# Kernel optimization log

Hardware: AMD Instinct MI355X
Metric: run time of the kernel (lower is better)

Reference implementation:

```python
import jax, jax.numpy as jnp
import numpy as np

B, N, D, H, DH = 4, 1024, 1024, 16, 64
INNER = H * DH  # 1024


def setup_inputs() -> dict:
    key = jax.random.key(0)
    k0, k1, k2, k3 = jax.random.split(key, 4)
    x = jax.random.normal(k0, (B, N, D), dtype=jnp.float32)
    # float 0/1 padding mask per token
    mask = jax.random.randint(k1, (B, N), 0, 2).astype(jnp.float32)
    w_qkv = jax.random.normal(k2, (D, 3 * INNER), dtype=jnp.float32) * (D ** -0.5)
    w_out = jax.random.normal(k3, (INNER, D), dtype=jnp.float32) * (INNER ** -0.5)
    b_out = jnp.zeros((D,), dtype=jnp.float32)
    return {"x": x, "mask": mask, "w_qkv": w_qkv, "w_out": w_out, "b_out": b_out}


def reference(x, mask, w_qkv, w_out, b_out):
    scale = DH ** -0.5
    qkv = x @ w_qkv  # [B,N,3*INNER]
    q, k, v = jnp.split(qkv, 3, axis=-1)
    resh = lambda t: t.reshape(B, N, H, DH).transpose(0, 2, 1, 3)  # b h n d
    q, k, v = resh(q), resh(k), resh(v)
    dots = jnp.einsum('bhnd,bhmd->bhnm', q, k) * scale  # [B,H,N,N]
    # attn_bias = 1 - m_i*m_j; blocked where isclose(attn_bias, 1) i.e. pair ~ 0
    pair = mask[:, None, :, None] * mask[:, None, None, :]  # [B,1,N,N]
    blocked = jnp.isclose(1.0 - pair, jnp.ones_like(pair))
    dots = jnp.where(blocked, -jnp.inf, dots)
    # fully-masked-row fixup: rows that are all -inf get dots=0, attn forced to 0
    valid = jnp.any(dots != -jnp.inf, axis=-1, keepdims=True)  # [B,H,N,1]
    dots = jnp.where(valid, dots, 0.0)
    attn = jax.nn.softmax(dots, axis=-1)
    attn = jnp.where(valid, attn, 0.0)
    out = jnp.einsum('bhnm,bhmd->bhnd', attn, v)
    out = out.transpose(0, 2, 1, 3).reshape(B, N, INNER)
    return out @ w_out + b_out
```

## Files before the change

kernel.cpp:

```cpp
#include <hip/hip_runtime.h>

#define INF __builtin_inff()

typedef __attribute__((ext_vector_type(8))) short bf16x8;
typedef __attribute__((ext_vector_type(4))) short s16x4;
typedef __attribute__((ext_vector_type(4))) float f32x4;
typedef __attribute__((ext_vector_type(8))) unsigned short u16x8;
typedef __attribute__((ext_vector_type(4))) unsigned short u16x4;

#define MFMA16(a, b, c) __builtin_amdgcn_mfma_f32_16x16x32_bf16(a, b, c, 0, 0, 0)

#define ASYNC16(g, l) __builtin_amdgcn_global_load_lds( \
    (const __attribute__((address_space(1))) unsigned int*)(const void*)(g), \
    (__attribute__((address_space(3))) unsigned int*)(void*)(l), 16, 0, 0)

__device__ __forceinline__ unsigned short f2bf(float f) {
  union { float f; unsigned u; } v; v.f = f;
  unsigned r = v.u + 0x7fffu + ((v.u >> 16) & 1u);
  return (unsigned short)(r >> 16);
}

__global__ __launch_bounds__(1024) void k_scan(
    const float* __restrict__ mask, unsigned short* __restrict__ perm, int* __restrict__ nv) {
  __shared__ int wsum[16];
  __shared__ int woff[16];
  const int b = blockIdx.x, t = threadIdx.x;
  const int wid = t >> 6, lane = t & 63;
  const bool valid = (mask[b * 1024 + t] != 0.f);
  unsigned long long bal = __ballot(valid);
  int pre = __popcll(bal & ((1ull << lane) - 1ull));
  if (lane == 0) wsum[wid] = __popcll(bal);
  __syncthreads();
  if (t < 16) { int s = 0; for (int i = 0; i < t; ++i) s += wsum[i]; woff[t] = s; }
  __syncthreads();
  const int nvt = woff[15] + wsum[15];
  const int p = woff[wid] + pre;
  perm[b * 1024 + (valid ? p : nvt + (t - p))] = (unsigned short)t;
  if (t == 0) nv[b] = nvt;
}

__global__ __launch_bounds__(256) void k_cvtg(
    const float* __restrict__ x, const unsigned short* __restrict__ perm,
    const int* __restrict__ nvb, unsigned short* __restrict__ xc) {
  const int id = blockIdx.x;
  const int b = id >> 10, slot = id & 1023;
  const int nv = nvb[b];
  if (slot >= ((nv + 127) & ~127)) return;
  const int t = threadIdx.x;
  u16x4 o;
  if (slot < nv) {
    int tok = perm[b * 1024 + slot];
    float4 f = ((const float4*)(x + ((size_t)(b * 1024 + tok)) * 1024))[t];
    o[0] = f2bf(f.x); o[1] = f2bf(f.y); o[2] = f2bf(f.z); o[3] = f2bf(f.w);
  } else {
    o[0] = o[1] = o[2] = o[3] = 0;
  }
  ((u16x4*)(xc + ((size_t)(b * 1024 + slot)) * 1024))[t] = o;
}

__global__ __launch_bounds__(256) void k_wtrans(
    const float* __restrict__ wqkv, const float* __restrict__ wout,
    unsigned short* __restrict__ wqkvt, unsigned short* __restrict__ woutt) {
  __shared__ float tile[32][33];
  int id = blockIdx.x;
  const float* src; unsigned short* dst; int C, bc, br;
  if (id < 3072) { src = wqkv;  dst = wqkvt; C = 3072; bc = (id % 96) * 32; br = (id / 96) * 32; }
  else { id -= 3072; src = wout; dst = woutt; C = 1024; bc = (id & 31) * 32; br = (id >> 5) * 32; }
  const int R = 1024;
  const int tx = threadIdx.x & 31, ty = threadIdx.x >> 5;
#pragma unroll
  for (int i = 0; i < 32; i += 8)
    tile[ty + i][tx] = src[(size_t)(br + ty + i) * C + bc + tx];
  __syncthreads();
#pragma unroll
  for (int i = 0; i < 32; i += 8)
    dst[(size_t)(bc + ty + i) * R + br + tx] = f2bf(tile[tx][ty + i]);
}

__global__ __launch_bounds__(256) void k_gemm_qkv(
    const unsigned short* __restrict__ A, const unsigned short* __restrict__ Bt,
    const int* __restrict__ nvb,
    unsigned short* __restrict__ qcmp, unsigned short* __restrict__ kcmp,
    unsigned short* __restrict__ vt) {
  __shared__ unsigned short SH[32768];
  const int lid = blockIdx.x;
  const int xcd = lid & 7, i6 = lid >> 3;
  const int colt = xcd * 3 + (i6 % 3);
  const int rowt = i6 / 3;
  const int b = rowt >> 3, mt = rowt & 7;
  const int nv = nvb[b];
  if (mt * 128 >= nv) return;
  const int bm0 = mt * 128;
  const int bn0 = colt * 128;
  const size_t abase = ((size_t)(b * 1024 + bm0)) * 1024;
  const int t = threadIdx.x;
  const int lane = t & 63, wave = t >> 6;
  const int wm = (wave >> 1) * 64, wn = (wave & 1) * 64;
  const int lr = lane & 15, quad = lane >> 4;
  const int sw = lr & 7;
  f32x4 acc[4][4] = {};
  auto stage = [&](int pp, int k0) {
    unsigned short* As = SH + pp * 16384;
    unsigned short* Bs = As + 8192;
#pragma unroll
    for (int j = 0; j < 4; ++j) {
      int idx = t + j * 256;
      int row = idx >> 3;
      int g = (idx ^ row) & 7;
      ASYNC16(&A[abase + (size_t)row * 1024 + k0 + g * 8], &As[idx * 8]);
      ASYNC16(&Bt[((size_t)(bn0 + row)) * 1024 + k0 + g * 8], &Bs[idx * 8]);
    }
  };
  stage(0, 0);
  for (int it = 0; it < 16; ++it) {
    const int pp = it & 1;
    __syncthreads();
    if (it + 1 < 16) stage(1 - pp, (it + 1) * 64);
    const unsigned short* As = SH + pp * 16384;
    const unsigned short* Bs = As + 8192;
#pragma unroll
    for (int ks = 0; ks < 2; ++ks) {
      bf16x8 af[4], bfr[4];
#pragma unroll
      for (int i = 0; i < 4; ++i)
        af[i] = *(const bf16x8*)(&As[(wm + i * 16 + lr) * 64 + (((ks * 4 + quad) ^ sw)) * 8]);
#pragma unroll
      for (int j = 0; j < 4; ++j)
        bfr[j] = *(const bf16x8*)(&Bs[(wn + j * 16 + lr) * 64 + (((ks * 4 + quad) ^ sw)) * 8]);
#pragma unroll
      for (int i = 0; i < 4; ++i)
#pragma unroll
        for (int j = 0; j < 4; ++j)
          acc[i][j] = MFMA16(af[i], bfr[j], acc[i][j]);
    }
  }
  const int sec = bn0 >> 10;
  const int js0 = bn0 & 1023;
#pragma unroll
  for (int hh = 0; hh < 2; ++hh) {
    __syncthreads();
    if ((wave >> 1) == hh) {
#pragma unroll
      for (int i = 0; i < 4; ++i)
#pragma unroll
        for (int j = 0; j < 4; ++j)
#pragma unroll
          for (int r = 0; r < 4; ++r)
            SH[(i * 16 + quad * 4 + r) * 136 + wn + j * 16 + lr] = f2bf(acc[i][j][r]);
    }
    __syncthreads();
    if (sec < 2) {
      unsigned short* dstT = sec ? kcmp : qcmp;
#pragma unroll
      for (int rr = 0; rr < 4; ++rr) {
        int lrow = (t >> 4) + rr * 16;
        int ck = t & 15;
        int slot = bm0 + hh * 64 + lrow;
        int js = js0 + ck * 8;
        int h = js >> 6, d = js & 63;
        u16x8 v = *(u16x8*)(&SH[lrow * 136 + ck * 8]);
        *(u16x8*)(&dstT[(((size_t)(b * 16 + h)) * 1024 + slot) * 64 + d]) = v;
      }
    } else {
      const int c = t & 127, seg = t >> 7;
      const int js = js0 + c, h = js >> 6, d = js & 63;
      unsigned short* vrow =
          &vt[(((size_t)(b * 16 + h)) * 64 + d) * 1024 + bm0 + hh * 64 + seg * 32];
#pragma unroll
      for (int s4 = 0; s4 < 4; ++s4) {
        u16x8 v;
#pragma unroll
        for (int s = 0; s < 8; ++s) v[s] = SH[(seg * 32 + s4 * 8 + s) * 136 + c];
        *(u16x8*)(vrow + s4 * 8) = v;
      }
    }
  }
}

__global__ __launch_bounds__(256, 3) void k_attn(
    const unsigned short* __restrict__ qcmp, const unsigned short* __restrict__ kcmp,
    const unsigned short* __restrict__ vtc, const int* __restrict__ nvb,
    unsigned short* __restrict__ aoc) {
  __shared__ unsigned short Ks[2][4096];
  __shared__ unsigned short Vs[2][4096];
  __shared__ unsigned short P[4][16 * 72];
  const int bx = blockIdx.x;
  const int bh = (bx & 7) + 8 * (bx >> 7);
  const int qcb = (bx >> 3) & 15;
  const int b = bh >> 4;
  const int nv = nvb[b];
  if (qcb * 64 >= nv) return;
  const int t = threadIdx.x;
  const int wave = t >> 6, lane = t & 63;
  const int lr = lane & 15, quad = lane >> 4;
  const int q0 = qcb * 64 + wave * 16;
  const unsigned short* qp = qcmp + ((size_t)bh << 16);
  const unsigned short* kp = kcmp + ((size_t)bh << 16);
  const unsigned short* vp = vtc + ((size_t)bh << 16);
  unsigned short* Pw = P[wave];
  bf16x8 qv0 = *(const bf16x8*)(qp + (q0 + lr) * 64 + quad * 8);
  bf16x8 qv1 = *(const bf16x8*)(qp + (q0 + lr) * 64 + 32 + quad * 8);
  float m = -INF, l = 0.f;
  f32x4 o[4] = {};
  const int sw = lr & 7;
  const int nk = (nv + 63) >> 6;
  auto stage = [&](int pp, int kc0) {
#pragma unroll
    for (int ld = 0; ld < 2; ++ld) {
      int idx = t + ld * 256;
      int row = idx >> 3;
      int g = (idx ^ row) & 7;
      ASYNC16(kp + (kc0 + row) * 64 + g * 8, &Ks[pp][idx * 8]);
      ASYNC16(vp + (size_t)row * 1024 + kc0 + g * 8, &Vs[pp][idx * 8]);
    }
  };
  stage(0, 0);
  for (int it = 0; it < nk; ++it) {
    const int pp = it & 1;
    const int kc0 = it * 64;
    __syncthreads();
    if (it + 1 < nk) stage(1 - pp, kc0 + 64);
    f32x4 st[4];
#pragma unroll
    for (int tt = 0; tt < 4; ++tt) {
      int krow = tt * 16 + lr;
      bf16x8 k0 = *(const bf16x8*)(&Ks[pp][krow * 64 + ((quad ^ sw)) * 8]);
      bf16x8 k1 = *(const bf16x8*)(&Ks[pp][krow * 64 + (((4 + quad) ^ sw)) * 8]);
      f32x4 c = {};
      c = MFMA16(k0, qv0, c);
      c = MFMA16(k1, qv1, c);
      st[tt] = c;
    }
    float tm = -INF;
#pragma unroll
    for (int tt = 0; tt < 4; ++tt) {
#pragma unroll
      for (int r = 0; r < 4; ++r) {
        int slot = kc0 + tt * 16 + quad * 4 + r;
        float v = (slot < nv) ? st[tt][r] * 0.125f : -INF;
        st[tt][r] = v;
        tm = fmaxf(tm, v);
      }
    }
    tm = fmaxf(tm, __shfl_xor(tm, 16));
    tm = fmaxf(tm, __shfl_xor(tm, 32));
    float mn = fmaxf(m, tm);
    float alpha = __expf(m - mn);
    if (m == -INF) alpha = 1.f;
    float ps = 0.f;
#pragma unroll
    for (int tt = 0; tt < 4; ++tt) {
      s16x4 pv;
#pragma unroll
      for (int r = 0; r < 4; ++r) {
        float pe = __expf(st[tt][r] - mn);
        ps += pe;
        pv[r] = (short)f2bf(pe);
      }
      *(s16x4*)(&Pw[lr * 72 + tt * 16 + quad * 4]) = pv;
    }
    ps += __shfl_xor(ps, 16);
    ps += __shfl_xor(ps, 32);
    l = l * alpha + ps;
    m = mn;
    float ar[4];
#pragma unroll
    for (int r = 0; r < 4; ++r) ar[r] = __shfl(alpha, quad * 4 + r);
#pragma unroll
    for (int jj = 0; jj < 4; ++jj)
#pragma unroll
      for (int r = 0; r < 4; ++r) o[jj][r] *= ar[r];
#pragma unroll
    for (int sh = 0; sh < 2; ++sh) {
      bf16x8 pa = *(const bf16x8*)(&Pw[lr * 72 + sh * 32 + quad * 8]);
#pragma unroll
      for (int jj = 0; jj < 4; ++jj) {
        bf16x8 vbf = *(const bf16x8*)(&Vs[pp][(jj * 16 + lr) * 64 + (((sh * 4 + quad) ^ sw)) * 8]);
        o[jj] = MFMA16(pa, vbf, o[jj]);
      }
    }
  }
  float inv = 1.f / l;
  float ir[4];
#pragma unroll
  for (int r = 0; r < 4; ++r) ir[r] = __shfl(inv, quad * 4 + r);
  const int h = bh & 15;
#pragma unroll
  for (int r = 0; r < 4; ++r) {
    int slot = q0 + quad * 4 + r;
    if (slot < nv) {
      size_t rowb = ((size_t)(b * 1024 + slot)) * 1024 + h * 64;
#pragma unroll
      for (int jj = 0; jj < 4; ++jj)
        aoc[rowb + jj * 16 + lr] = f2bf(o[jj][r] * ir[r]);
    }
  }
}

__global__ __launch_bounds__(256) void k_biasfill(
    const float* __restrict__ bias, const unsigned short* __restrict__ perm,
    const int* __restrict__ nvb, float* __restrict__ out) {
  const int b = blockIdx.x >> 10, slot = blockIdx.x & 1023;
  if (slot < nvb[b]) return;
  const int tok = perm[b * 1024 + slot];
  ((float4*)(out + ((size_t)(b * 1024 + tok)) * 1024))[threadIdx.x] =
      ((const float4*)bias)[threadIdx.x];
}

__global__ __launch_bounds__(256) void k_gemm_out(
    const unsigned short* __restrict__ A, const unsigned short* __restrict__ Bt,
    const unsigned short* __restrict__ perm, const int* __restrict__ nvb,
    const float* __restrict__ bias, float* __restrict__ C) {
  __shared__ unsigned short SH[24576];
  const int lid = blockIdx.x;
  const int col = lid & 7;
  const int rt = lid >> 3;
  const int b = rt >> 4, mt = rt & 15;
  const int nv = nvb[b];
  if (mt * 64 >= nv) return;
  const int bm0 = mt * 64;
  const int bn0 = col * 128;
  const size_t abase = ((size_t)(b * 1024 + bm0)) * 1024;
  const int t = threadIdx.x;
  const int lane = t & 63, wave = t >> 6;
  const int wm = (wave >> 1) * 32, wn = (wave & 1) * 64;
  const int lr = lane & 15, quad = lane >> 4;
  const int sw = lr & 7;
  f32x4 acc[2][4] = {};
  auto stage = [&](int pp, int k0) {
    unsigned short* As = SH + pp * 12288;
    unsigned short* Bs = As + 4096;
#pragma unroll
    for (int j = 0; j < 2; ++j) {
      int idx = t + j * 256;
      int row = idx >> 3;
      int g = (idx ^ row) & 7;
      ASYNC16(&A[abase + (size_t)row * 1024 + k0 + g * 8], &As[idx * 8]);
    }
#pragma unroll
    for (int j = 0; j < 4; ++j) {
      int idx = t + j * 256;
      int row = idx >> 3;
      int g = (idx ^ row) & 7;
      ASYNC16(&Bt[((size_t)(bn0 + row)) * 1024 + k0 + g * 8], &Bs[idx * 8]);
    }
  };
  stage(0, 0);
  for (int it = 0; it < 16; ++it) {
    const int pp = it & 1;
    __syncthreads();
    if (it + 1 < 16) stage(1 - pp, (it + 1) * 64);
    const unsigned short* As = SH + pp * 12288;
    const unsigned short* Bs = As + 4096;
#pragma unroll
    for (int ks = 0; ks < 2; ++ks) {
      bf16x8 af[2], bfr[4];
#pragma unroll
      for (int i = 0; i < 2; ++i)
        af[i] = *(const bf16x8*)(&As[(wm + i * 16 + lr) * 64 + (((ks * 4 + quad) ^ sw)) * 8]);
#pragma unroll
      for (int j = 0; j < 4; ++j)
        bfr[j] = *(const bf16x8*)(&Bs[(wn + j * 16 + lr) * 64 + (((ks * 4 + quad) ^ sw)) * 8]);
#pragma unroll
      for (int i = 0; i < 2; ++i)
#pragma unroll
        for (int j = 0; j < 4; ++j)
          acc[i][j] = MFMA16(af[i], bfr[j], acc[i][j]);
    }
  }
#pragma unroll
  for (int i = 0; i < 2; ++i)
#pragma unroll
    for (int r = 0; r < 4; ++r) {
      int slot = bm0 + wm + i * 16 + quad * 4 + r;
      if (slot < nv) {
        int tok = perm[b * 1024 + slot];
        size_t rowb = ((size_t)(b * 1024 + tok)) * 1024;
#pragma unroll
        for (int j = 0; j < 4; ++j) {
          int c = bn0 + wn + j * 16 + lr;
          C[rowb + c] = acc[i][j][r] + bias[c];
        }
      }
    }
}

extern "C" void kernel_launch(void* const* d_in, const int* in_sizes, int n_in,
                              void* d_out, int out_size, void* d_ws, size_t ws_size,
                              hipStream_t stream) {
  const float* x    = (const float*)d_in[0];
  const float* mask = (const float*)d_in[1];
  const float* wqkv = (const float*)d_in[2];
  const float* wout = (const float*)d_in[3];
  const float* bout = (const float*)d_in[4];
  float* out = (float*)d_out;
  char* ws = (char*)d_ws;
  unsigned short* xc    = (unsigned short*)(ws);
  unsigned short* aoc   = (unsigned short*)(ws);
  unsigned short* wqkvt = (unsigned short*)(ws + (size_t)( 8 << 20));
  unsigned short* woutt = (unsigned short*)(ws + (size_t)(14 << 20));
  unsigned short* qcmp  = (unsigned short*)(ws + (size_t)(16 << 20));
  unsigned short* kcmp  = (unsigned short*)(ws + (size_t)(24 << 20));
  unsigned short* vt    = (unsigned short*)(ws + (size_t)(32 << 20));
  unsigned short* perm  = (unsigned short*)(ws + (size_t)(40 << 20));
  int*            nvb   = (int*)           (ws + (size_t)(40 << 20) + 8192);

  k_scan<<<4, 1024, 0, stream>>>(mask, perm, nvb);
  k_cvtg<<<4096, 256, 0, stream>>>(x, perm, nvb, xc);
  k_wtrans<<<4096, 256, 0, stream>>>(wqkv, wout, wqkvt, woutt);
  k_gemm_qkv<<<768, 256, 0, stream>>>(xc, wqkvt, nvb, qcmp, kcmp, vt);
  k_attn<<<1024, 256, 0, stream>>>(qcmp, kcmp, vt, nvb, aoc);
  k_biasfill<<<4096, 256, 0, stream>>>(bout, perm, nvb, out);
  k_gemm_out<<<512, 256, 0, stream>>>(aoc, woutt, perm, nvb, bout, out);
}
```

Baseline: 149.1 us.

## Fuse mask scan, input gather and weight transpose into one prep kernel; fold bias fill into output GEMM

Merges the scan, gather-convert and weight-transpose kernels into a single launch. Each gather block recomputes the per-batch compaction in shared memory, so it no longer has to wait for a separate scan kernel. The bias-fill for masked tokens moves into extra blocks of the output GEMM launch. Together this cuts the pipeline from seven launches to four, removing launch gaps and serialization. The cost is redundant scan work in every gather block and some divergent block roles sharing a launch.

```diff
diff --git a/kernel.cpp b/kernel.cpp
--- a/kernel.cpp
+++ b/kernel.cpp
@@ -20,61 +20,84 @@
   return (unsigned short)(r >> 16);
 }
 
-__global__ __launch_bounds__(1024) void k_scan(
-    const float* __restrict__ mask, unsigned short* __restrict__ perm, int* __restrict__ nv) {
-  __shared__ int wsum[16];
-  __shared__ int woff[16];
-  const int b = blockIdx.x, t = threadIdx.x;
-  const int wid = t >> 6, lane = t & 63;
-  const bool valid = (mask[b * 1024 + t] != 0.f);
-  unsigned long long bal = __ballot(valid);
-  int pre = __popcll(bal & ((1ull << lane) - 1ull));
-  if (lane == 0) wsum[wid] = __popcll(bal);
+__global__ __launch_bounds__(256) void k_prep(
+    const float* __restrict__ x, const float* __restrict__ mask,
+    const float* __restrict__ wqkv, const float* __restrict__ wout,
+    unsigned short* __restrict__ xc, unsigned short* __restrict__ wqkvt,
+    unsigned short* __restrict__ woutt, unsigned short* __restrict__ perm,
+    int* __restrict__ nvb) {
+  __shared__ union {
+    float tile[32][33];
+    struct { unsigned short lperm[1024]; int wtot[4]; } sc;
+  } sh;
+  const int lid = blockIdx.x;
+  const int t = threadIdx.x, lane = t & 63, wid = t >> 6;
+
+  if (lid >= 4 && lid < 4100) {
+    int id = lid - 4;
+    const float* src; unsigned short* dst; int C, bc, br;
+    if (id < 3072) { src = wqkv; dst = wqkvt; C = 3072; bc = (id % 96) * 32; br = (id / 96) * 32; }
+    else { id -= 3072; src = wout; dst = woutt; C = 1024; bc = (id & 31) * 32; br = (id >> 5) * 32; }
+    const int tx = t & 31, ty = t >> 5;
+#pragma unroll
+    for (int i = 0; i < 32; i += 8)
+      sh.tile[ty + i][tx] = src[(size_t)(br + ty + i) * C + bc + tx];
+    __syncthreads();
+#pragma unroll
+    for (int i = 0; i < 32; i += 8)
+      dst[(size_t)(bc + ty + i) * 1024 + br + tx] = f2bf(sh.tile[tx][ty + i]);
+    return;
+  }
+
+  const int b = (lid < 4) ? lid : ((lid - 4100) >> 8);
+  float4 mv = ((const float4*)(mask + b * 1024))[t];
+  int v0 = mv.x != 0.f, v1 = mv.y != 0.f, v2 = mv.z != 0.f, v3 = mv.w != 0.f;
+  int cnt = v0 + v1 + v2 + v3;
+  int pre = cnt;
+#pragma unroll
+  for (int d = 1; d < 64; d <<= 1) { int n = __shfl_up(pre, d); if (lane >= d) pre += n; }
+  if (lane == 63) sh.sc.wtot[wid] = pre;
   __syncthreads();
-  if (t < 16) { int s = 0; for (int i = 0; i < t; ++i) s += wsum[i]; woff[t] = s; }
+  int base = 0;
+#pragma unroll
+  for (int i = 0; i < 4; ++i) if (i < wid) base += sh.sc.wtot[i];
+  const int nvt = sh.sc.wtot[0] + sh.sc.wtot[1] + sh.sc.wtot[2] + sh.sc.wtot[3];
+  int ex = base + pre - cnt;
+  int vv[4] = { v0, v1, v2, v3 };
+
+  if (lid < 4) {
+#pragma unroll
+    for (int j = 0; j < 4; ++j) {
+      int tok = t * 4 + j;
+      if (vv[j]) { perm[b * 1024 + ex] = (unsigned short)tok; ++ex; }
+      else         perm[b * 1024 + nvt + (tok - ex)] = (unsigned short)tok;
+    }
+    if (t == 0) nvb[b] = nvt;
+    return;
+  }
+
+#pragma unroll
+  for (int j = 0; j < 4; ++j) {
+    int tok = t * 4 + j;
+    if (vv[j]) { sh.sc.lperm[ex] = (unsigned short)tok; ++ex; }
+  }
   __syncthreads();
-  const int nvt = woff[15] + wsum[15];
-  const int p = woff[wid] + pre;
-  perm[b * 1024 + (valid ? p : nvt + (t - p))] = (unsigned short)t;
-  if (t == 0) nv[b] = nvt;
-}
-
-__global__ __launch_bounds__(256) void k_cvtg(
-    const float* __restrict__ x, const unsigned short* __restrict__ perm,
-    const int* __restrict__ nvb, unsigned short* __restrict__ xc) {
-  const int id = blockIdx.x;
-  const int b = id >> 10, slot = id & 1023;
-  const int nv = nvb[b];
-  if (slot >= ((nv + 127) & ~127)) return;
-  const int t = threadIdx.x;
-  u16x4 o;
-  if (slot < nv) {
-    int tok = perm[b * 1024 + slot];
-    float4 f = ((const float4*)(x + ((size_t)(b * 1024 + tok)) * 1024))[t];
-    o[0] = f2bf(f.x); o[1] = f2bf(f.y); o[2] = f2bf(f.z); o[3] = f2bf(f.w);
-  } else {
-    o[0] = o[1] = o[2] = o[3] = 0;
-  }
-  ((u16x4*)(xc + ((size_t)(b * 1024 + slot)) * 1024))[t] = o;
-}
-
-__global__ __launch_bounds__(256) void k_wtrans(
-    const float* __restrict__ wqkv, const float* __restrict__ wout,
-    unsigned short* __restrict__ wqkvt, unsigned short* __restrict__ woutt) {
-  __shared__ float tile[32][33];
-  int id = blockIdx.x;
-  const float* src; unsigned short* dst; int C, bc, br;
-  if (id < 3072) { src = wqkv;  dst = wqkvt; C = 3072; bc = (id % 96) * 32; br = (id / 96) * 32; }
-  else { id -= 3072; src = wout; dst = woutt; C = 1024; bc = (id & 31) * 32; br = (id >> 5) * 32; }
-  const int R = 1024;
-  const int tx = threadIdx.x & 31, ty = threadIdx.x >> 5;
-#pragma unroll
-  for (int i = 0; i < 32; i += 8)
-    tile[ty + i][tx] = src[(size_t)(br + ty + i) * C + bc + tx];
-  __syncthreads();
-#pragma unroll
-  for (int i = 0; i < 32; i += 8)
-    dst[(size_t)(bc + ty + i) * R + br + tx] = f2bf(tile[tx][ty + i]);
+  const int s0 = ((lid - 4100) & 255) * 4;
+  const int ce = (nvt + 127) & ~127;
+#pragma unroll
+  for (int j = 0; j < 4; ++j) {
+    int slot = s0 + j;
+    if (slot >= ce) continue;
+    u16x4 o;
+    if (slot < nvt) {
+      int tok = sh.sc.lperm[slot];
+      float4 f = ((const float4*)(x + ((size_t)(b * 1024 + tok)) * 1024))[t];
+      o[0] = f2bf(f.x); o[1] = f2bf(f.y); o[2] = f2bf(f.z); o[3] = f2bf(f.w);
+    } else {
+      o[0] = o[1] = o[2] = o[3] = 0;
+    }
+    ((u16x4*)(xc + ((size_t)(b * 1024 + slot)) * 1024))[t] = o;
+  }
 }
 
 __global__ __launch_bounds__(256) void k_gemm_qkv(
@@ -297,22 +320,30 @@
   }
 }
 
-__global__ __launch_bounds__(256) void k_biasfill(
-    const float* __restrict__ bias, const unsigned short* __restrict__ perm,
-    const int* __restrict__ nvb, float* __restrict__ out) {
-  const int b = blockIdx.x >> 10, slot = blockIdx.x & 1023;
-  if (slot < nvb[b]) return;
-  const int tok = perm[b * 1024 + slot];
-  ((float4*)(out + ((size_t)(b * 1024 + tok)) * 1024))[threadIdx.x] =
-      ((const float4*)bias)[threadIdx.x];
-}
-
-__global__ __launch_bounds__(256) void k_gemm_out(
+__global__ __launch_bounds__(256) void k_gemm_fin(
     const unsigned short* __restrict__ A, const unsigned short* __restrict__ Bt,
     const unsigned short* __restrict__ perm, const int* __restrict__ nvb,
     const float* __restrict__ bias, float* __restrict__ C) {
   __shared__ unsigned short SH[24576];
   const int lid = blockIdx.x;
+  const int t = threadIdx.x;
+  if (lid >= 512) {
+    const int idx = lid - 512;
+    const int b = idx >> 6, ch = idx & 63;
+    const int nv = nvb[b];
+    const float4 bv = ((const float4*)bias)[t];
+    for (int s = nv + ch * 8; s < 1024; s += 512) {
+#pragma unroll
+      for (int j = 0; j < 8; ++j) {
+        int slot = s + j;
+        if (slot < 1024) {
+          int tok = perm[b * 1024 + slot];
+          ((float4*)(C + ((size_t)(b * 1024 + tok)) * 1024))[t] = bv;
+        }
+      }
+    }
+    return;
+  }
   const int col = lid & 7;
   const int rt = lid >> 3;
   const int b = rt >> 4, mt = rt & 15;
@@ -321,7 +352,6 @@
   const int bm0 = mt * 64;
   const int bn0 = col * 128;
   const size_t abase = ((size_t)(b * 1024 + bm0)) * 1024;
-  const int t = threadIdx.x;
   const int lane = t & 63, wave = t >> 6;
   const int wm = (wave >> 1) * 32, wn = (wave & 1) * 64;
   const int lr = lane & 15, quad = lane >> 4;
@@ -405,11 +435,8 @@
   unsigned short* perm  = (unsigned short*)(ws + (size_t)(40 << 20));
   int*            nvb   = (int*)           (ws + (size_t)(40 << 20) + 8192);
 
-  k_scan<<<4, 1024, 0, stream>>>(mask, perm, nvb);
-  k_cvtg<<<4096, 256, 0, stream>>>(x, perm, nvb, xc);
-  k_wtrans<<<4096, 256, 0, stream>>>(wqkv, wout, wqkvt, woutt);
+  k_prep<<<5124, 256, 0, stream>>>(x, mask, wqkv, wout, xc, wqkvt, woutt, perm, nvb);
   k_gemm_qkv<<<768, 256, 0, stream>>>(xc, wqkvt, nvb, qcmp, kcmp, vt);
   k_attn<<<1024, 256, 0, stream>>>(qcmp, kcmp, vt, nvb, aoc);
-  k_biasfill<<<4096, 256, 0, stream>>>(bout, perm, nvb, out);
-  k_gemm_out<<<512, 256, 0, stream>>>(aoc, woutt, perm, nvb, bout, out);
-}
+  k_gemm_fin<<<768, 256, 0, stream>>>(aoc, woutt, perm, nvb, bout, out);
+}
```

Result: faster. 145.6 us (-2.4%).
